# Kernel optimization log

Hardware: AMD Instinct MI355X
Metric: run time of the kernel (lower is better)

## Reference

```python
import math
import jax, jax.numpy as jnp
import numpy as np

N_HEAD = 16

def setup_inputs() -> dict:
    key = jax.random.key(0)
    k1, k2, k3 = jax.random.split(key, 3)
    B, T, C = 2, 2048, 1024
    x = jax.random.normal(k1, (B, T, C), dtype=jnp.float32)
    w_attn = jax.random.normal(k2, (C, 3 * C), dtype=jnp.float32) * (1.0 / math.sqrt(C))
    b_attn = jnp.zeros((3 * C,), dtype=jnp.float32)
    w_proj = jax.random.normal(k3, (C, C), dtype=jnp.float32) * (1.0 / math.sqrt(C))
    b_proj = jnp.zeros((C,), dtype=jnp.float32)
    return {"x": x, "w_attn": w_attn, "b_attn": b_attn, "w_proj": w_proj, "b_proj": b_proj}

def reference(x, w_attn, b_attn, w_proj, b_proj):
    B, T, C = x.shape
    H = N_HEAD
    D = C // H
    qkv = x @ w_attn + b_attn                       # [B,T,3C]
    q, k, v = jnp.split(qkv, 3, axis=-1)
    # [B,T,C] -> [B,H,T,D]
    q = q.reshape(B, T, H, D).transpose(0, 2, 1, 3)
    k = k.reshape(B, T, H, D).transpose(0, 2, 1, 3)
    v = v.reshape(B, T, H, D).transpose(0, 2, 1, 3)
    scores = jnp.einsum("bhtd,bhsd->bhts", q, k) * (1.0 / math.sqrt(D))  # [B,H,T,T]
    causal = jnp.tril(jnp.ones((T, T), dtype=bool))
    scores = jnp.where(causal, scores, jnp.finfo(scores.dtype).min)
    attn = jax.nn.softmax(scores, axis=-1)
    y = jnp.einsum("bhts,bhsd->bhtd", attn, v)      # [B,H,T,D]
    y = y.transpose(0, 2, 1, 3).reshape(B, T, C)
    return y @ w_proj + b_proj
```

## Files before the change

kernel.cpp:

```cpp
#include <hip/hip_runtime.h>
#include <stdint.h>

#define BB 2
#define TT 2048
#define CCx 1024
#define HH 16
#define DD 64
#define MM (BB*TT)
#define C3 (3*CCx)

using u16 = unsigned short;
typedef __attribute__((ext_vector_type(8))) short short8;
typedef __attribute__((ext_vector_type(4))) float f32x4;
typedef __attribute__((ext_vector_type(16))) float f32x16;

__device__ __forceinline__ float bf2f(u16 u){
  union { unsigned int i; float f; } v; v.i = ((unsigned int)u) << 16; return v.f;
}
__device__ __forceinline__ u16 f2bf(float f){
  union { float f; unsigned int u; } v; v.f = f;
  unsigned int r = v.u + 0x7fffu + ((v.u >> 16) & 1u);
  return (u16)(r >> 16);
}

__device__ __forceinline__ f32x4 mfma16x16x32(short8 a, short8 b, f32x4 c){
  return __builtin_amdgcn_mfma_f32_16x16x32_bf16(a, b, c, 0, 0, 0);
}
__device__ __forceinline__ f32x16 mfma32x32x16(short8 a, short8 b, f32x16 c){
  return __builtin_amdgcn_mfma_f32_32x32x16_bf16(a, b, c, 0, 0, 0);
}

typedef __attribute__((address_space(1))) unsigned int gu32;
typedef __attribute__((address_space(3))) unsigned int su32;
__device__ __forceinline__ void gload16(const void* g, void* l){
  __builtin_amdgcn_global_load_lds((gu32*)g, (su32*)l, 16, 0, 0);
}

__global__ __launch_bounds__(256) void cvt_x_k(const float* __restrict__ inv,
                                               u16* __restrict__ out, int n8){
  int i = blockIdx.x*256 + threadIdx.x;
  if (i >= n8) return;
  const float* p = inv + (size_t)i*8;
  float4 a = *(const float4*)p, b = *(const float4*)(p+4);
  short8 v;
  v[0]=(short)f2bf(a.x); v[1]=(short)f2bf(a.y); v[2]=(short)f2bf(a.z); v[3]=(short)f2bf(a.w);
  v[4]=(short)f2bf(b.x); v[5]=(short)f2bf(b.y); v[6]=(short)f2bf(b.z); v[7]=(short)f2bf(b.w);
  *(short8*)(out + (size_t)i*8) = v;
}

__global__ __launch_bounds__(256) void transpose_cvt_k(const float* __restrict__ inv,
                                                       u16* __restrict__ out,
                                                       int R, int Cc){
  __shared__ u16 t[64][65];
  const int bx = blockIdx.x*64, by = blockIdx.y*64;
  const int tx = threadIdx.x & 63, ty = threadIdx.x >> 6;
  #pragma unroll
  for (int i = 0; i < 16; ++i){
    int r = ty + i*4;
    t[r][tx] = f2bf(inv[(size_t)(by+r)*Cc + bx+tx]);
  }
  __syncthreads();
  #pragma unroll
  for (int i = 0; i < 16; ++i){
    int r = ty + i*4;
    out[(size_t)(bx+r)*R + by+tx] = t[tx][r];
  }
}

__global__ __launch_bounds__(256) void gemm_nt(const u16* __restrict__ A,
                                               const u16* __restrict__ BT,
                                               const float* __restrict__ bias,
                                               void* __restrict__ Cmat,
                                               int M, int N, int K, int of32){
  __shared__ u16 lA[128*64];
  __shared__ u16 lB[128*64];
  const int tid  = threadIdx.x;
  const int lane = tid & 63;
  const int wave = tid >> 6;
  const int nwg = gridDim.x * gridDim.y;
  const int lin = blockIdx.y * gridDim.x + blockIdx.x;
  const int wg  = (lin & 7) * (nwg >> 3) + (lin >> 3);
  const int bm = wg % gridDim.x, bn = wg / gridDim.x;
  const int wm = (wave >> 1) * 64;
  const int wn = (wave & 1) * 64;
  const int ln15 = lane & 15, g = lane >> 4;

  f32x4 acc[4][4];
  #pragma unroll
  for (int i = 0; i < 4; ++i)
    #pragma unroll
    for (int j = 0; j < 4; ++j) acc[i][j] = (f32x4){0.f,0.f,0.f,0.f};

  const int trow = tid >> 3;
  const int tc8s = (tid & 7) ^ (trow & 7);
  const size_t arow0 = (size_t)(bm*128) * K;
  const size_t brow0 = (size_t)(bn*128) * K;

  for (int k0 = 0; k0 < K; k0 += 64) {
    __syncthreads();
    #pragma unroll
    for (int c = 0; c < 4; ++c) {
      const int row = c*32 + trow;
      const size_t roff = (size_t)row*K + k0 + tc8s*8;
      gload16(A + arow0 + roff, (char*)lA + (c*256 + (wave<<6))*16);
      gload16(BT + brow0 + roff, (char*)lB + (c*256 + (wave<<6))*16);
    }
    asm volatile("s_waitcnt vmcnt(0)" ::: "memory");
    __syncthreads();

    short8 af[4][2], bfr[4][2];
    #pragma unroll
    for (int mf = 0; mf < 4; ++mf)
      #pragma unroll
      for (int kc = 0; kc < 2; ++kc) {
        const int r = wm + mf*16 + ln15;
        const int cb = (kc*64 + (g << 4)) ^ ((r & 7) << 4);
        af[mf][kc] = *(const short8*)((const char*)lA + r*128 + cb);
      }
    #pragma unroll
    for (int nf = 0; nf < 4; ++nf)
      #pragma unroll
      for (int kc = 0; kc < 2; ++kc) {
        const int r = wn + nf*16 + ln15;
        const int cb = (kc*64 + (g << 4)) ^ ((r & 7) << 4);
        bfr[nf][kc] = *(const short8*)((const char*)lB + r*128 + cb);
      }
    #pragma unroll
    for (int kc = 0; kc < 2; ++kc)
      #pragma unroll
      for (int mf = 0; mf < 4; ++mf)
        #pragma unroll
        for (int nf = 0; nf < 4; ++nf)
          acc[mf][nf] = mfma16x16x32(af[mf][kc], bfr[nf][kc], acc[mf][nf]);
  }

  #pragma unroll
  for (int nf = 0; nf < 4; ++nf) {
    const int col = bn*128 + wn + nf*16 + ln15;
    const float bv = bias[col];
    #pragma unroll
    for (int mf = 0; mf < 4; ++mf) {
      #pragma unroll
      for (int r = 0; r < 4; ++r) {
        const int rowg = bm*128 + wm + mf*16 + g*4 + r;
        const float v = acc[mf][nf][r] + bv;
        if (of32) ((float*)Cmat)[(size_t)rowg*N + col] = v;
        else      ((u16*)Cmat)[(size_t)rowg*N + col] = f2bf(v);
      }
    }
  }
}

#define LOG2E_S 0.1803369f
__global__ __launch_bounds__(256, 2) void attn_k(const u16* __restrict__ qkv,
                                                 u16* __restrict__ y){
  __shared__ u16 kb[2][64*64];
  __shared__ u16 vb[2][64*64];
  const int tid  = threadIdx.x;
  const int lane = tid & 63;
  const int wave = tid >> 6;
  const int jq = 15 - blockIdx.x;
  const int bh = blockIdx.y;
  const int b = bh >> 4, h = bh & 15;
  const int l31 = lane & 31;
  const int hw  = lane >> 5;
  const int q0w = jq*128 + wave*32;
  const int myq = q0w + l31;
  const int ntw = 2*jq + (wave >> 1) + 1;
  const int nt  = 2*jq + 2;
  const size_t base = (size_t)b * TT * C3;

  const int krw = tid >> 3;
  const int tc8 = (tid & 7) ^ (krw & 7);
  const u16* ksrc = qkv + base + CCx + h*DD + tc8*8 + (size_t)krw*C3;
  const int vkey = tid >> 3, vc8 = tid & 7;
  const u16* vsrc = qkv + base + 2*CCx + h*DD + (size_t)vkey*C3 + vc8*8;

  short8 qf[4];
  {
    const u16* qp = qkv + base + (size_t)myq*C3 + h*DD + hw*8;
    #pragma unroll
    for (int dk = 0; dk < 4; ++dk) qf[dk] = *(const short8*)(qp + 16*dk);
  }

  f32x16 o0, o1;
  #pragma unroll
  for (int i = 0; i < 16; ++i){ o0[i] = 0.f; o1[i] = 0.f; }
  float m = -1e30f, lsum = 0.f;

  short8 vr0, vr1;
  #define KSTAGE(curb, kv0v) do { \
    const u16* kp_ = ksrc + (size_t)(kv0v)*C3; \
    char* kd_ = (char*)kb + (curb)*8192 + wave*1024; \
    gload16(kp_, kd_); \
    gload16(kp_ + (size_t)32*C3, kd_ + 4096); \
  } while(0)
  #define VLOAD(kv0v) do { \
    vr0 = *(const short8*)(vsrc + (size_t)(kv0v)*C3); \
    vr1 = *(const short8*)(vsrc + (size_t)(kv0v + 32)*C3); \
  } while(0)
  #define VSTORE(curb) do { \
    char* vd_ = (char*)vb + (curb)*8192; \
    _Pragma("unroll") \
    for (int i = 0; i < 8; ++i){ \
      const int d_ = vc8*8 + i; \
      const int sw_ = (i + vc8) & 7; \
      *(u16*)(vd_ + d_*128 + (((vkey>>3) ^ sw_) << 4) + (vkey & 7)*2) = (u16)vr0[i]; \
      *(u16*)(vd_ + d_*128 + ((((vkey+32)>>3) ^ sw_) << 4) + (vkey & 7)*2) = (u16)vr1[i]; \
    } \
  } while(0)

  KSTAGE(0, 0);
  VLOAD(0);
  asm volatile("s_waitcnt vmcnt(0)" ::: "memory");
  VSTORE(0);
  __syncthreads();

  int cur = 0;
  for (int t = 0; t < nt; ++t){
    const int kv0 = t*64;
    const bool hn = (t + 1 < nt);
    if (hn){ KSTAGE(cur^1, kv0 + 64); VLOAD(kv0 + 64); }

    if (t < ntw){
      const char* kbc = (const char*)kb + cur*8192;
      f32x16 s0, s1;
      #pragma unroll
      for (int i = 0; i < 16; ++i){ s0[i] = 0.f; s1[i] = 0.f; }
      #pragma unroll
      for (int dk = 0; dk < 4; ++dk){
        const int chunk = 2*dk + hw;
        const int r0 = l31, r1 = 32 + l31;
        short8 k0 = *(const short8*)(kbc + r0*128 + ((chunk ^ (r0 & 7)) << 4));
        short8 k1 = *(const short8*)(kbc + r1*128 + ((chunk ^ (r1 & 7)) << 4));
        s0 = mfma32x32x16(k0, qf[dk], s0);
        s1 = mfma32x32x16(k1, qf[dk], s1);
      }

      float tmax = -1e30f;
      #pragma unroll
      for (int r = 0; r < 16; ++r){
        const int key0 = kv0 + (r & 3) + 8*(r >> 2) + 4*hw;
        s0[r] = (key0      <= myq) ? s0[r] : -1e30f;
        s1[r] = (key0 + 32 <= myq) ? s1[r] : -1e30f;
        tmax = fmaxf(tmax, fmaxf(s0[r], s1[r]));
      }
      tmax = fmaxf(tmax, __shfl_xor(tmax, 32));

      if (__any(tmax > m + 64.f)){
        const float nm = fmaxf(m, tmax);
        const float fac = exp2f((m - nm) * LOG2E_S);
        m = nm; lsum *= fac;
        #pragma unroll
        for (int r = 0; r < 16; ++r){
          const int qrow = (r & 3) + 8*(r >> 2) + 4*hw;
          const float fr = __shfl(fac, qrow);
          o0[r] *= fr; o1[r] *= fr;
        }
      }

      const float mscl = m * LOG2E_S;
      float rsum = 0.f;
      unsigned wpk0[2][4], wpk1[2][4];
      #pragma unroll
      for (int bq = 0; bq < 4; ++bq){
        float p00 = exp2f(fmaf(s0[4*bq+0], LOG2E_S, -mscl));
        float p01 = exp2f(fmaf(s0[4*bq+1], LOG2E_S, -mscl));
        float p02 = exp2f(fmaf(s0[4*bq+2], LOG2E_S, -mscl));
        float p03 = exp2f(fmaf(s0[4*bq+3], LOG2E_S, -mscl));
        float p10 = exp2f(fmaf(s1[4*bq+0], LOG2E_S, -mscl));
        float p11 = exp2f(fmaf(s1[4*bq+1], LOG2E_S, -mscl));
        float p12 = exp2f(fmaf(s1[4*bq+2], LOG2E_S, -mscl));
        float p13 = exp2f(fmaf(s1[4*bq+3], LOG2E_S, -mscl));
        rsum += (p00+p01) + (p02+p03) + (p10+p11) + (p12+p13);
        asm("v_cvt_pk_bf16_f32 %0, %1, %2" : "=v"(wpk0[0][bq]) : "v"(p00), "v"(p01));
        asm("v_cvt_pk_bf16_f32 %0, %1, %2" : "=v"(wpk1[0][bq]) : "v"(p02), "v"(p03));
        asm("v_cvt_pk_bf16_f32 %0, %1, %2" : "=v"(wpk0[1][bq]) : "v"(p10), "v"(p11));
        asm("v_cvt_pk_bf16_f32 %0, %1, %2" : "=v"(wpk1[1][bq]) : "v"(p12), "v"(p13));
      }
      lsum += rsum + __shfl_xor(rsum, 32);

      short8 pa[4];
      #pragma unroll
      for (int kt = 0; kt < 2; ++kt)
        #pragma unroll
        for (int j = 0; j < 2; ++j){
          const unsigned ownA  = hw ? wpk0[kt][2*j+1] : wpk0[kt][2*j];
          const unsigned ownB  = hw ? wpk1[kt][2*j+1] : wpk1[kt][2*j];
          const unsigned sendA = hw ? wpk0[kt][2*j]   : wpk0[kt][2*j+1];
          const unsigned sendB = hw ? wpk1[kt][2*j]   : wpk1[kt][2*j+1];
          const unsigned recvA = (unsigned)__shfl_xor((int)sendA, 32);
          const unsigned recvB = (unsigned)__shfl_xor((int)sendB, 32);
          union { unsigned u[4]; short8 s8; } pu;
          pu.u[0] = hw ? recvA : ownA;
          pu.u[1] = hw ? recvB : ownB;
          pu.u[2] = hw ? ownA : recvA;
          pu.u[3] = hw ? ownB : recvB;
          pa[2*kt + j] = pu.s8;
        }

      const char* vbc = (const char*)vb + cur*8192;
      const int d0 = l31,      sw0 = ((d0 & 7) + ((d0 >> 3) & 7)) & 7;
      const int d1 = 32 + l31, sw1 = ((d1 & 7) + ((d1 >> 3) & 7)) & 7;
      #pragma unroll
      for (int ks = 0; ks < 4; ++ks){
        const int chunk = 2*ks + hw;
        short8 v0 = *(const short8*)(vbc + d0*128 + ((chunk ^ sw0) << 4));
        short8 v1 = *(const short8*)(vbc + d1*128 + ((chunk ^ sw1) << 4));
        o0 = mfma32x32x16(pa[ks], v0, o0);
        o1 = mfma32x32x16(pa[ks], v1, o1);
      }
    }

    if (hn){
      asm volatile("s_waitcnt vmcnt(0)" ::: "memory");
      VSTORE(cur^1);
    }
    __syncthreads();
    cur ^= 1;
  }

  const float inv = 1.0f / lsum;
  #pragma unroll
  for (int r = 0; r < 16; ++r){
    const int qrow = (r & 3) + 8*(r >> 2) + 4*hw;
    const float ir = __shfl(inv, qrow);
    const size_t row = (size_t)(b*TT + q0w + qrow)*CCx + h*DD;
    y[row + l31]      = f2bf(o0[r] * ir);
    y[row + 32 + l31] = f2bf(o1[r] * ir);
  }
  #undef KSTAGE
  #undef VLOAD
  #undef VSTORE
}

extern "C" void kernel_launch(void* const* d_in, const int* in_sizes, int n_in,
                              void* d_out, int out_size, void* d_ws, size_t ws_size,
                              hipStream_t stream) {
  const float *x = nullptr, *w_attn = nullptr, *b_attn = nullptr,
              *w_proj = nullptr, *b_proj = nullptr;
  for (int i = 0; i < n_in; ++i) {
    switch (in_sizes[i]) {
      case MM*CCx:  x      = (const float*)d_in[i]; break;
      case C3*CCx:  w_attn = (const float*)d_in[i]; break;
      case C3:      b_attn = (const float*)d_in[i]; break;
      case CCx*CCx: w_proj = (const float*)d_in[i]; break;
      case CCx:     b_proj = (const float*)d_in[i]; break;
    }
  }
  float* out = (float*)d_out;

  char* ws = (char*)d_ws;
  u16* xb      = (u16*)ws;
  u16* wT_attn = xb + (size_t)MM*CCx;
  u16* wT_proj = wT_attn + (size_t)C3*CCx;
  u16* qkv     = wT_proj + (size_t)CCx*CCx;
  u16* ybuf    = qkv + (size_t)MM*C3;

  cvt_x_k<<<(MM*CCx/8 + 255)/256, 256, 0, stream>>>(x, xb, MM*CCx/8);
  transpose_cvt_k<<<dim3(C3/64, CCx/64), 256, 0, stream>>>(w_attn, wT_attn, CCx, C3);
  transpose_cvt_k<<<dim3(CCx/64, CCx/64), 256, 0, stream>>>(w_proj, wT_proj, CCx, CCx);
  gemm_nt<<<dim3(MM/128, C3/128), 256, 0, stream>>>(xb, wT_attn, b_attn, qkv, MM, C3, CCx, 0);
  attn_k<<<dim3(16, BB*HH), 256, 0, stream>>>(qkv, ybuf);
  gemm_nt<<<dim3(MM/128, CCx/128), 256, 0, stream>>>(ybuf, wT_proj, b_proj, out, MM, CCx, CCx, 1);
}
```

Measured before the change: 159.7 us.

## Split attention KV range across wave pairs with LDS merge and 64-row query tiles

Each block now handles 64 query rows instead of 128, and the grid doubles to 32 blocks per head. The two waves of each pair process alternate KV tiles, which split-K style, and merge their softmax partial state through shared memory at the end. The shared-memory ring grows to four K/V tiles so two tiles can be prefetched per step. Causal masking now runs only on the diagonal tile, and block order is interleaved to balance load. The price is doubled LDS use, which may reduce occupancy, plus extra merge work and an extra barrier.

```diff
diff --git a/kernel.cpp b/kernel.cpp
--- a/kernel.cpp
+++ b/kernel.cpp
@@ -154,20 +154,25 @@
 #define LOG2E_S 0.1803369f
 __global__ __launch_bounds__(256, 2) void attn_k(const u16* __restrict__ qkv,
                                                  u16* __restrict__ y){
-  __shared__ u16 kb[2][64*64];
-  __shared__ u16 vb[2][64*64];
+  __shared__ u16 kb[4][64*64];
+  __shared__ u16 vb[4][64*64];
   const int tid  = threadIdx.x;
   const int lane = tid & 63;
   const int wave = tid >> 6;
-  const int jq = 15 - blockIdx.x;
+  const int bx = blockIdx.x;
+  const int cc = bx & 7, jj = bx >> 3;
+  const int jt = (jj == 0) ? (31 - cc) : (jj == 1) ? (16 + cc)
+               : (jj == 2) ? (15 - cc) : cc;
   const int bh = blockIdx.y;
   const int b = bh >> 4, h = bh & 15;
   const int l31 = lane & 31;
   const int hw  = lane >> 5;
-  const int q0w = jq*128 + wave*32;
+  const int qs  = wave >> 1;
+  const int par = wave & 1;
+  const int q0w = jt*64 + qs*32;
   const int myq = q0w + l31;
-  const int ntw = 2*jq + (wave >> 1) + 1;
-  const int nt  = 2*jq + 2;
+  const int nt  = jt + 1;
+  const int nsteps = (nt + 1) >> 1;
   const size_t base = (size_t)b * TT * C3;
 
   const int krw = tid >> 3;
@@ -188,42 +193,47 @@
   for (int i = 0; i < 16; ++i){ o0[i] = 0.f; o1[i] = 0.f; }
   float m = -1e30f, lsum = 0.f;
 
-  short8 vr0, vr1;
-  #define KSTAGE(curb, kv0v) do { \
-    const u16* kp_ = ksrc + (size_t)(kv0v)*C3; \
-    char* kd_ = (char*)kb + (curb)*8192 + wave*1024; \
+  short8 vrA0, vrA1, vrB0, vrB1;
+  #define KSTAGE(tile) do { \
+    const u16* kp_ = ksrc + (size_t)(tile)*64*C3; \
+    char* kd_ = (char*)kb + (((tile)&3) << 13) + wave*1024; \
     gload16(kp_, kd_); \
     gload16(kp_ + (size_t)32*C3, kd_ + 4096); \
   } while(0)
-  #define VLOAD(kv0v) do { \
-    vr0 = *(const short8*)(vsrc + (size_t)(kv0v)*C3); \
-    vr1 = *(const short8*)(vsrc + (size_t)(kv0v + 32)*C3); \
-  } while(0)
-  #define VSTORE(curb) do { \
-    char* vd_ = (char*)vb + (curb)*8192; \
+  #define VLOADA(tile) do { const u16* vp_ = vsrc + (size_t)(tile)*64*C3; \
+    vrA0 = *(const short8*)vp_; vrA1 = *(const short8*)(vp_ + (size_t)32*C3); } while(0)
+  #define VLOADB(tile) do { const u16* vp_ = vsrc + (size_t)(tile)*64*C3; \
+    vrB0 = *(const short8*)vp_; vrB1 = *(const short8*)(vp_ + (size_t)32*C3); } while(0)
+  #define VSTORE(tile, r0_, r1_) do { \
+    char* vd_ = (char*)vb + (((tile)&3) << 13); \
     _Pragma("unroll") \
     for (int i = 0; i < 8; ++i){ \
       const int d_ = vc8*8 + i; \
       const int sw_ = (i + vc8) & 7; \
-      *(u16*)(vd_ + d_*128 + (((vkey>>3) ^ sw_) << 4) + (vkey & 7)*2) = (u16)vr0[i]; \
-      *(u16*)(vd_ + d_*128 + ((((vkey+32)>>3) ^ sw_) << 4) + (vkey & 7)*2) = (u16)vr1[i]; \
+      *(u16*)(vd_ + d_*128 + (((vkey>>3) ^ sw_) << 4) + (vkey & 7)*2) = (u16)r0_[i]; \
+      *(u16*)(vd_ + d_*128 + ((((vkey+32)>>3) ^ sw_) << 4) + (vkey & 7)*2) = (u16)r1_[i]; \
     } \
   } while(0)
 
-  KSTAGE(0, 0);
-  VLOAD(0);
+  KSTAGE(0);
+  VLOADA(0);
+  if (nt > 1){ KSTAGE(1); VLOADB(1); }
   asm volatile("s_waitcnt vmcnt(0)" ::: "memory");
-  VSTORE(0);
+  VSTORE(0, vrA0, vrA1);
+  if (nt > 1) VSTORE(1, vrB0, vrB1);
   __syncthreads();
 
-  int cur = 0;
-  for (int t = 0; t < nt; ++t){
-    const int kv0 = t*64;
-    const bool hn = (t + 1 < nt);
-    if (hn){ KSTAGE(cur^1, kv0 + 64); VLOAD(kv0 + 64); }
-
-    if (t < ntw){
-      const char* kbc = (const char*)kb + cur*8192;
+  for (int ti = 0; ti < nsteps; ++ti){
+    const int t0 = 2*ti;
+    const int pf0 = t0 + 2, pf1 = t0 + 3;
+    const bool hp0 = pf0 < nt, hp1 = pf1 < nt;
+    if (hp0){ KSTAGE(pf0); VLOADA(pf0); }
+    if (hp1){ KSTAGE(pf1); VLOADB(pf1); }
+
+    const int tt = t0 + par;
+    if (tt < nt){
+      const int kv0 = tt*64;
+      const char* kbc = (const char*)kb + ((tt&3) << 13);
       f32x16 s0, s1;
       #pragma unroll
       for (int i = 0; i < 16; ++i){ s0[i] = 0.f; s1[i] = 0.f; }
@@ -238,12 +248,18 @@
       }
 
       float tmax = -1e30f;
-      #pragma unroll
-      for (int r = 0; r < 16; ++r){
-        const int key0 = kv0 + (r & 3) + 8*(r >> 2) + 4*hw;
-        s0[r] = (key0      <= myq) ? s0[r] : -1e30f;
-        s1[r] = (key0 + 32 <= myq) ? s1[r] : -1e30f;
-        tmax = fmaxf(tmax, fmaxf(s0[r], s1[r]));
+      if (tt == jt){
+        #pragma unroll
+        for (int r = 0; r < 16; ++r){
+          const int key0 = kv0 + (r & 3) + 8*(r >> 2) + 4*hw;
+          s0[r] = (key0      <= myq) ? s0[r] : -1e30f;
+          s1[r] = (key0 + 32 <= myq) ? s1[r] : -1e30f;
+          tmax = fmaxf(tmax, fmaxf(s0[r], s1[r]));
+        }
+      } else {
+        #pragma unroll
+        for (int r = 0; r < 16; ++r)
+          tmax = fmaxf(tmax, fmaxf(s0[r], s1[r]));
       }
       tmax = fmaxf(tmax, __shfl_xor(tmax, 32));
 
@@ -299,7 +315,7 @@
           pa[2*kt + j] = pu.s8;
         }
 
-      const char* vbc = (const char*)vb + cur*8192;
+      const char* vbc = (const char*)vb + ((tt&3) << 13);
       const int d0 = l31,      sw0 = ((d0 & 7) + ((d0 >> 3) & 7)) & 7;
       const int d1 = 32 + l31, sw1 = ((d1 & 7) + ((d1 >> 3) & 7)) & 7;
       #pragma unroll
@@ -312,25 +328,46 @@
       }
     }
 
-    if (hn){
+    if (hp0){
       asm volatile("s_waitcnt vmcnt(0)" ::: "memory");
-      VSTORE(cur^1);
-    }
+      VSTORE(pf0, vrA0, vrA1);
+    }
+    if (hp1) VSTORE(pf1, vrB0, vrB1);
     __syncthreads();
-    cur ^= 1;
-  }
-
-  const float inv = 1.0f / lsum;
-  #pragma unroll
-  for (int r = 0; r < 16; ++r){
-    const int qrow = (r & 3) + 8*(r >> 2) + 4*hw;
-    const float ir = __shfl(inv, qrow);
-    const size_t row = (size_t)(b*TT + q0w + qrow)*CCx + h*DD;
-    y[row + l31]      = f2bf(o0[r] * ir);
-    y[row + 32 + l31] = f2bf(o1[r] * ir);
+  }
+
+  float* mg = (float*)kb + (size_t)qs*2112;
+  if (par){
+    #pragma unroll
+    for (int r = 0; r < 16; ++r){
+      const int qrow = (r & 3) + 8*(r >> 2) + 4*hw;
+      mg[qrow*64 + l31]      = o0[r];
+      mg[qrow*64 + 32 + l31] = o1[r];
+    }
+    if (hw == 0){ mg[2048 + l31] = m; mg[2080 + l31] = lsum; }
+  }
+  __syncthreads();
+  if (!par){
+    const float m1 = mg[2048 + l31];
+    const float l1 = mg[2080 + l31];
+    const float M  = fmaxf(m, m1);
+    const float f0 = exp2f((m  - M) * LOG2E_S);
+    const float f1 = exp2f((m1 - M) * LOG2E_S);
+    const float iv = 1.0f / (lsum*f0 + l1*f1);
+    #pragma unroll
+    for (int r = 0; r < 16; ++r){
+      const int qrow = (r & 3) + 8*(r >> 2) + 4*hw;
+      const float ir  = __shfl(iv, qrow);
+      const float f0r = __shfl(f0, qrow);
+      const float f1r = __shfl(f1, qrow);
+      const size_t row = (size_t)(b*TT + q0w + qrow)*CCx + h*DD;
+      y[row + l31]      = f2bf((o0[r]*f0r + mg[qrow*64 + l31]*f1r) * ir);
+      y[row + 32 + l31] = f2bf((o1[r]*f0r + mg[qrow*64 + 32 + l31]*f1r) * ir);
+    }
   }
   #undef KSTAGE
-  #undef VLOAD
+  #undef VLOADA
+  #undef VLOADB
   #undef VSTORE
 }
 
@@ -361,6 +398,6 @@
   transpose_cvt_k<<<dim3(C3/64, CCx/64), 256, 0, stream>>>(w_attn, wT_attn, CCx, C3);
   transpose_cvt_k<<<dim3(CCx/64, CCx/64), 256, 0, stream>>>(w_proj, wT_proj, CCx, CCx);
   gemm_nt<<<dim3(MM/128, C3/128), 256, 0, stream>>>(xb, wT_attn, b_attn, qkv, MM, C3, CCx, 0);
-  attn_k<<<dim3(16, BB*HH), 256, 0, stream>>>(qkv, ybuf);
+  attn_k<<<dim3(32, BB*HH), 256, 0, stream>>>(qkv, ybuf);
   gemm_nt<<<dim3(MM/128, CCx/128), 256, 0, stream>>>(ybuf, wT_proj, b_proj, out, MM, CCx, CCx, 1);
 }
```

Result: slower. 170.9 us (+7.0%).
